# Optimization experiments

Hardware: AMD Instinct MI355X
Metric: run time of the kernel (lower is better)

The kernel has to match this reference:

```python
import jax, jax.numpy as jnp
import numpy as np

# --- Cl(3,0,1) projective geometric algebra structure constants (GATr blade order) ---
BLADES = [(), (0,), (1,), (2,), (3,), (0, 1), (0, 2), (0, 3), (1, 2), (1, 3), (2, 3),
          (0, 1, 2), (0, 1, 3), (0, 2, 3), (1, 2, 3), (0, 1, 2, 3)]
IDX = {b: i for i, b in enumerate(BLADES)}
METRIC = [0.0, 1.0, 1.0, 1.0]  # e0 degenerate, e1,e2,e3 square to +1


def _mul_blades(a, b):
    """Multiply two basis blades; returns (sign, sorted_blade_tuple)."""
    lst = list(a) + list(b)
    sign = 1.0
    changed = True
    while changed:
        changed = False
        k = 0
        while k < len(lst) - 1:
            if lst[k] > lst[k + 1]:
                lst[k], lst[k + 1] = lst[k + 1], lst[k]
                sign = -sign
                changed = True
            elif lst[k] == lst[k + 1]:
                sign *= METRIC[lst[k]]
                del lst[k:k + 2]
                changed = True
            else:
                k += 1
    return sign, tuple(lst)


def _tables():
    gp = np.zeros((16, 16, 16), np.float32)
    outer = np.zeros((16, 16, 16), np.float32)
    for j, bj in enumerate(BLADES):
        for k, bk in enumerate(BLADES):
            s, bl = _mul_blades(bj, bk)
            if s != 0.0:
                gp[IDX[bl], j, k] = s
            if set(bj).isdisjoint(bk):  # outer product: nonzero only for disjoint blades
                outer[IDX[bl], j, k] = s
    # dual map D: blade -> signed complement, with blade ^ complement = sign * e0123
    D = np.zeros((16, 16), np.float32)
    for j, bj in enumerate(BLADES):
        comp = tuple(i for i in range(4) if i not in bj)
        s, _ = _mul_blades(bj, comp)
        D[IDX[comp], j] = s
    # join(x, y) = dual(dual(x) ^ dual(y))  ->  bilinear tensor [16,16,16]
    join = np.einsum('ai,ijk,jb,kc->abc', D, outer, D, D).astype(np.float32)
    # Pin-equivariant linear basis: 5 grade projections + 4 e0-wedge-per-grade maps
    grades = np.array([len(b) for b in BLADES])
    basis = np.zeros((9, 16, 16), np.float32)
    for g in range(5):
        basis[g] = np.diag((grades == g).astype(np.float32))
    e0_mul = outer[:, IDX[(0,)], :]  # x -> e0 ^ x
    for g in range(4):
        basis[5 + g] = e0_mul * (grades == g)[None, :].astype(np.float32)
    return gp, join, basis


B, N = 8, 4096
IN_MV, HID, OUT_MV = 32, 32, 32
HALF = HID // 2
IN_S, OUT_S = 64, 64
NB = 9


def setup_inputs() -> dict:
    key = jax.random.key(0)
    ks = jax.random.split(key, 16)
    gp, jn, basis = _tables()

    def wmv(k, o, i):
        return jax.random.normal(k, (o, i, NB), jnp.float32) / np.sqrt(i * NB)

    def ws(k, o, i):
        return jax.random.normal(k, (o, i), jnp.float32) / np.sqrt(i)

    return dict(
        multivectors=jax.random.normal(ks[0], (B, N, IN_MV, 16), jnp.float32),
        reference_mv=jax.random.normal(ks[1], (B, N, 16), jnp.float32),
        scalars=jax.random.normal(ks[2], (B, N, IN_S), jnp.float32),
        basis=jnp.asarray(basis), gp=jnp.asarray(gp), jn=jnp.asarray(jn),
        w_left_mv=wmv(ks[3], HALF, IN_MV), w_left_s=ws(ks[4], HALF, IN_S),
        w_right_mv=wmv(ks[5], HALF, IN_MV), w_right_s=ws(ks[6], HALF, IN_S),
        w_jl_mv=wmv(ks[7], HALF, IN_MV), w_jl_s=ws(ks[8], HALF, IN_S),
        w_jr_mv=wmv(ks[9], HALF, IN_MV), w_jr_s=ws(ks[10], HALF, IN_S),
        w_out_mv=wmv(ks[11], OUT_MV, HID), w_out_s2mv=ws(ks[12], OUT_MV, IN_S),
        w_out_mvs2s=ws(ks[13], OUT_S, HID), w_out_s2s=ws(ks[14], OUT_S, IN_S),
    )


def _equi_linear(x, s, w_mv, w_s, basis):
    # fold the 9 equivariant basis maps into the channel-mixing weight once (tiny)
    W = jnp.einsum('oib,bjk->oijk', w_mv, basis)  # [out, in, 16, 16]
    out = jnp.einsum('oijk,...ik->...oj', W, x)   # (..., out, 16)
    # scalar inputs feed the multivector scalar component (blade index 0)
    out = out.at[..., 0].add(jnp.einsum('os,...s->...o', w_s, s))
    return out


def reference(multivectors, reference_mv, scalars, basis, gp, jn,
              w_left_mv, w_left_s, w_right_mv, w_right_s, w_jl_mv, w_jl_s,
              w_jr_mv, w_jr_s, w_out_mv, w_out_s2mv, w_out_mvs2s, w_out_s2s):
    left = _equi_linear(multivectors, scalars, w_left_mv, w_left_s, basis)
    right = _equi_linear(multivectors, scalars, w_right_mv, w_right_s, basis)
    gp_out = jnp.einsum('ijk,...cj,...ck->...ci', gp, left, right)  # geometric product

    jl = _equi_linear(multivectors, scalars, w_jl_mv, w_jl_s, basis)
    jr = _equi_linear(multivectors, scalars, w_jr_mv, w_jr_s, basis)
    # equivariant join, scaled by pseudoscalar (e0123) component of the reference
    join_out = jnp.einsum('ijk,...cj,...ck->...ci', jn, jl, jr) * reference_mv[..., None, 15:16]

    hidden = jnp.concatenate([gp_out, join_out], axis=-2)  # (..., HID, 16)
    out_mv = _equi_linear(hidden, scalars, w_out_mv, w_out_s2mv, basis)
    out_s = jnp.einsum('oc,...c->...o', w_out_mvs2s, hidden[..., 0]) \
        + jnp.einsum('os,...s->...o', w_out_s2s, scalars)
    return out_mv, out_s
```

## Files before the change

kernel.cpp:

```cpp
#include <hip/hip_runtime.h>
#include <stdint.h>


#define NPOS_TOTAL 32768

typedef __attribute__((ext_vector_type(8))) short short8;
typedef __attribute__((ext_vector_type(4))) float f32x4;
#define MFMA16(a,b,c) __builtin_amdgcn_mfma_f32_16x16x32_bf16((a),(b),(c),0,0,0)

constexpr int BLADE_MASK[16] = {0,1,2,4,8,3,5,9,6,10,12,7,11,13,14,15};
constexpr int MASK2IDX[16]   = {0,1,2,5,3,6,8,11,4,7,9,12,10,13,14,15};

struct MulRes { int sign; int mask; };

constexpr MulRes mul_blades(int ma, int mb) {
  int lst[8] = {0,0,0,0,0,0,0,0};
  int n = 0;
  for (int g = 0; g < 4; ++g) if ((ma >> g) & 1) lst[n++] = g;
  for (int g = 0; g < 4; ++g) if ((mb >> g) & 1) lst[n++] = g;
  int sign = 1;
  bool changed = true;
  while (changed) {
    changed = false;
    int k = 0;
    while (k + 1 < n) {
      if (lst[k] > lst[k+1]) {
        int t = lst[k]; lst[k] = lst[k+1]; lst[k+1] = t;
        sign = -sign; changed = true;
      } else if (lst[k] == lst[k+1]) {
        if (lst[k] == 0) sign = 0;
        for (int m = k; m + 2 < n; ++m) lst[m] = lst[m+2];
        n -= 2; changed = true;
      } else {
        ++k;
      }
    }
  }
  int mask = 0;
  for (int m = 0; m < n; ++m) mask |= (1 << lst[m]);
  if (sign == 0) mask = 0;
  return MulRes{sign, mask};
}

struct Tables {
  float gp_sgn[16][16]; int gp_idx[16][16];
  float jn_sgn[16][16]; int jn_idx[16][16];
  constexpr Tables() : gp_sgn{}, gp_idx{}, jn_sgn{}, jn_idx{} {
    for (int j = 0; j < 16; ++j) {
      for (int k = 0; k < 16; ++k) {
        MulRes r = mul_blades(BLADE_MASK[j], BLADE_MASK[k]);
        gp_sgn[j][k] = (float)r.sign;
        gp_idx[j][k] = MASK2IDX[r.mask & 15];
        jn_sgn[j][k] = 0.0f; jn_idx[j][k] = 0;
        int mb = BLADE_MASK[j], mc = BLADE_MASK[k];
        if ((mb | mc) == 15) {
          int cb = 15 ^ mb, cc = 15 ^ mc;
          MulRes sb = mul_blades(mb, cb);
          MulRes sc = mul_blades(mc, cc);
          MulRes ro = mul_blades(cb, cc);
          int imask = ro.mask;
          int amask = 15 ^ imask;
          MulRes si = mul_blades(imask, amask);
          jn_sgn[j][k] = (float)(si.sign * ro.sign * sb.sign * sc.sign);
          jn_idx[j][k] = MASK2IDX[amask & 15];
        }
      }
    }
  }
};
constexpr Tables TBL{};

constexpr int GRADE[16] = {0,1,1,1,1,2,2,2,2,2,2,3,3,3,3,4};
constexpr int E0_TGT[8]  = {1,5,6,7,11,12,13,15};
constexpr int E0_SRC[8]  = {0,2,3,4,8,9,10,14};
constexpr int E0_SLOT[8] = {5,6,6,6,7,7,7,8};

__device__ __forceinline__ float bflo(unsigned u) { return __uint_as_float(u << 16); }
__device__ __forceinline__ float bfhi(unsigned u) { return __uint_as_float(u & 0xffff0000u); }
__device__ __forceinline__ unsigned pk2(float a, float b) {
  unsigned ua = __float_as_uint(a), ub = __float_as_uint(b);
  unsigned ra = (ua + 0x7fffu + ((ua >> 16) & 1u)) >> 16;
  unsigned rb = (ub + 0x7fffu + ((ub >> 16) & 1u)) >> 16;
  return (ra & 0xffffu) | ((rb & 0xffffu) << 16);
}
__device__ __forceinline__ unsigned short bf1(float a) {
  unsigned ua = __float_as_uint(a);
  return (unsigned short)((ua + 0x7fffu + ((ua >> 16) & 1u)) >> 16);
}

__global__ void gb_prep(const float* __restrict__ wlmv, const float* __restrict__ wrmv,
                        const float* __restrict__ wjlmv, const float* __restrict__ wjrmv,
                        const float* __restrict__ wls,  const float* __restrict__ wrs,
                        const float* __restrict__ wjls, const float* __restrict__ wjrs,
                        const float* __restrict__ womv, const float* __restrict__ ws2mv,
                        const float* __restrict__ wm2s, const float* __restrict__ ws2s,
                        uint4* __restrict__ wpk) {
  int t = blockIdx.x * 256 + threadIdx.x;
  if (t >= 168 * 64) return;
  int blk = t >> 6, l = t & 63;
  int m = l & 15, q = l >> 4;
  float v[8];
  if (blk < 104) {
    int mat = blk >> 2, ot = blk & 3;
    const float* wmv[4] = {wlmv, wrmv, wjlmv, wjrmv};
    const float* wsc[4] = {wls, wrs, wjls, wjrs};
    for (int jj = 0; jj < 8; ++jj) {
      int k = q * 8 + jj;
      if (mat < 16)      v[jj] = wmv[ot][m * 288 + k * 9 + GRADE[mat]];
      else if (mat < 24) v[jj] = wmv[ot][m * 288 + k * 9 + E0_SLOT[mat - 16]];
      else               v[jj] = wsc[ot][m * 64 + (mat - 24) * 32 + k];
    }
  } else if (blk < 156) {
    int b2 = blk - 104, mat = b2 >> 1, ot = b2 & 1;
    int o = ot * 16 + m;
    for (int jj = 0; jj < 8; ++jj) {
      int k = q * 8 + jj;
      if (mat < 16)      v[jj] = womv[o * 288 + k * 9 + GRADE[mat]];
      else if (mat < 24) v[jj] = womv[o * 288 + k * 9 + E0_SLOT[mat - 16]];
      else               v[jj] = ws2mv[o * 64 + (mat - 24) * 32 + k];
    }
  } else {
    int b4 = blk - 156;
    for (int jj = 0; jj < 8; ++jj) {
      int k = q * 8 + jj;
      if (b4 < 4) { int o = b4 * 16 + m; v[jj] = wm2s[o * 32 + k]; }
      else { int half = (b4 - 4) >> 2, ot = (b4 - 4) & 3; int o = ot * 16 + m;
             v[jj] = ws2s[o * 64 + half * 32 + k]; }
    }
  }
  uint4 u;
  u.x = pk2(v[0], v[1]); u.y = pk2(v[2], v[3]);
  u.z = pk2(v[4], v[5]); u.w = pk2(v[6], v[7]);
  wpk[t] = u;
}

__global__ __launch_bounds__(256) void gb_main(
    const float* __restrict__ mv, const float* __restrict__ ref,
    const float* __restrict__ s, const uint4* __restrict__ wpk,
    float* __restrict__ out_mv, float* __restrict__ out_s) {
  __shared__ __align__(16) char smem[57600];
  unsigned short* xs_e = (unsigned short*)smem;
  unsigned*       xs_w = (unsigned*)smem;
  unsigned short* hl_e = (unsigned short*)smem;
  unsigned short* yl_e = (unsigned short*)(smem + 16640);
  unsigned*       yl_w = (unsigned*)(smem + 16640);

  const int tid  = threadIdx.x;
  const int wave = tid >> 6, lane = tid & 63;
  const int lm = lane & 15, lq = lane >> 4;
  const int P0 = blockIdx.x * 16;

  const float4* mv4 = (const float4*)mv + (size_t)P0 * 128;
  #pragma unroll
  for (int kk = 0; kk < 4; ++kk) {
    int e = tid + kk * 256;
    int p = e >> 6, sub = e & 63, i2 = sub >> 2, jg = sub & 3;
    float4 fa = mv4[p * 128 + i2 * 8 + jg];
    float4 fb = mv4[p * 128 + i2 * 8 + 4 + jg];
    int base = p * 260 + jg * 4 * 16 + i2;
    xs_w[base + 0 * 16] = pk2(fa.x, fb.x);
    xs_w[base + 1 * 16] = pk2(fa.y, fb.y);
    xs_w[base + 2 * 16] = pk2(fa.z, fb.z);
    xs_w[base + 3 * 16] = pk2(fa.w, fb.w);
  }

  short8 sfrag[2];
  {
    const float4* s4 = (const float4*)s + ((size_t)(P0 + lm)) * 16;
    #pragma unroll
    for (int h = 0; h < 2; ++h) {
      float4 a = s4[h * 8 + lq * 2];
      float4 b = s4[h * 8 + lq * 2 + 1];
      uint4 u;
      u.x = pk2(a.x, a.y); u.y = pk2(a.z, a.w);
      u.z = pk2(b.x, b.y); u.w = pk2(b.z, b.w);
      sfrag[h] = __builtin_bit_cast(short8, u);
    }
  }
  __syncthreads();

  {
    short8 bx[16];
    #pragma unroll
    for (int c = 0; c < 16; ++c)
      bx[c] = *(const short8*)&xs_e[lm * 520 + c * 32 + lq * 8];
    f32x4 zf = {0.f, 0.f, 0.f, 0.f};
    f32x4 acc[16];
    #pragma unroll
    for (int j = 0; j < 16; ++j) acc[j] = zf;
    #pragma unroll
    for (int j = 0; j < 16; ++j) {
      short8 w = __builtin_bit_cast(short8, wpk[(j * 4 + wave) * 64 + lane]);
      acc[j] = MFMA16(w, bx[j], acc[j]);
    }
    #pragma unroll
    for (int m = 0; m < 8; ++m) {
      short8 w = __builtin_bit_cast(short8, wpk[((16 + m) * 4 + wave) * 64 + lane]);
      acc[E0_TGT[m]] = MFMA16(w, bx[E0_SRC[m]], acc[E0_TGT[m]]);
    }
    #pragma unroll
    for (int h = 0; h < 2; ++h) {
      short8 w = __builtin_bit_cast(short8, wpk[((24 + h) * 4 + wave) * 64 + lane]);
      acc[0] = MFMA16(w, sfrag[h], acc[0]);
    }
    #pragma unroll
    for (int jp = 0; jp < 8; ++jp) {
      #pragma unroll
      for (int r = 0; r < 4; ++r) {
        int o = wave * 16 + lq * 4 + r;
        yl_w[o * 160 + lm * 10 + jp] = pk2(acc[2 * jp][r], acc[2 * jp + 1][r]);
      }
    }
  }
  __syncthreads();

  {
    const int pos = tid & 15;
    const int hc  = tid >> 4;
    const float rs = ref[(size_t)(P0 + pos) * 16 + 15];
    float L[16], R[16], H[16];
    auto ldrow = [&](int row, float* dst) {
      const unsigned short* p = yl_e + row * 320 + pos * 20;
      uint2 a = *(const uint2*)(p);
      uint2 b = *(const uint2*)(p + 4);
      uint2 c = *(const uint2*)(p + 8);
      uint2 d = *(const uint2*)(p + 12);
      unsigned uu[8] = {a.x, a.y, b.x, b.y, c.x, c.y, d.x, d.y};
      #pragma unroll
      for (int q = 0; q < 8; ++q) { dst[2*q] = bflo(uu[q]); dst[2*q+1] = bfhi(uu[q]); }
    };
    ldrow(hc, L); ldrow(16 + hc, R);
    #pragma unroll
    for (int q = 0; q < 16; ++q) H[q] = 0.f;
    #pragma unroll
    for (int j = 0; j < 16; ++j)
      #pragma unroll
      for (int k = 0; k < 16; ++k)
        if (TBL.gp_sgn[j][k] != 0.0f)
          H[TBL.gp_idx[j][k]] += TBL.gp_sgn[j][k] * L[j] * R[k];
    #pragma unroll
    for (int j = 0; j < 16; ++j)
      hl_e[pos * 520 + j * 32 + hc] = bf1(H[j]);
    ldrow(32 + hc, L); ldrow(48 + hc, R);
    #pragma unroll
    for (int q = 0; q < 16; ++q) { H[q] = 0.f; L[q] *= rs; }
    #pragma unroll
    for (int j = 0; j < 16; ++j)
      #pragma unroll
      for (int k = 0; k < 16; ++k)
        if (TBL.jn_sgn[j][k] != 0.0f)
          H[TBL.jn_idx[j][k]] += TBL.jn_sgn[j][k] * L[j] * R[k];
    #pragma unroll
    for (int j = 0; j < 16; ++j)
      hl_e[pos * 520 + j * 32 + 16 + hc] = bf1(H[j]);
  }
  __syncthreads();

  if (wave < 2) {
    short8 bh[16];
    #pragma unroll
    for (int j = 0; j < 16; ++j)
      bh[j] = *(const short8*)&hl_e[lm * 520 + j * 32 + lq * 8];
    f32x4 zf = {0.f, 0.f, 0.f, 0.f};
    f32x4 a3[16];
    #pragma unroll
    for (int j = 0; j < 16; ++j) a3[j] = zf;
    #pragma unroll
    for (int j = 0; j < 16; ++j) {
      short8 w = __builtin_bit_cast(short8, wpk[(104 + j * 2 + wave) * 64 + lane]);
      a3[j] = MFMA16(w, bh[j], a3[j]);
    }
    #pragma unroll
    for (int m = 0; m < 8; ++m) {
      short8 w = __builtin_bit_cast(short8, wpk[(104 + (16 + m) * 2 + wave) * 64 + lane]);
      a3[E0_TGT[m]] = MFMA16(w, bh[E0_SRC[m]], a3[E0_TGT[m]]);
    }
    #pragma unroll
    for (int h = 0; h < 2; ++h) {
      short8 w = __builtin_bit_cast(short8, wpk[(104 + (24 + h) * 2 + wave) * 64 + lane]);
      a3[0] = MFMA16(w, sfrag[h], a3[0]);
    }
    float* ob = out_mv + ((size_t)(P0 + lm)) * 512 + (size_t)(wave * 16 + lq * 4) * 16;
    #pragma unroll
    for (int r = 0; r < 4; ++r) {
      #pragma unroll
      for (int g = 0; g < 4; ++g) {
        *(float4*)(ob + r * 16 + g * 4) =
            make_float4(a3[4*g][r], a3[4*g+1][r], a3[4*g+2][r], a3[4*g+3][r]);
      }
    }
  } else {
    short8 bh0 = *(const short8*)&hl_e[lm * 520 + lq * 8];
    int w2 = wave - 2;
    f32x4 zf = {0.f, 0.f, 0.f, 0.f};
    #pragma unroll
    for (int t2 = 0; t2 < 2; ++t2) {
      int otg = w2 * 2 + t2;
      f32x4 aS = zf;
      aS = MFMA16(__builtin_bit_cast(short8, wpk[(156 + otg) * 64 + lane]), bh0, aS);
      aS = MFMA16(__builtin_bit_cast(short8, wpk[(160 + otg) * 64 + lane]), sfrag[0], aS);
      aS = MFMA16(__builtin_bit_cast(short8, wpk[(164 + otg) * 64 + lane]), sfrag[1], aS);
      float* osb = out_s + ((size_t)(P0 + lm)) * 64 + otg * 16 + lq * 4;
      *(float4*)osb = make_float4(aS[0], aS[1], aS[2], aS[3]);
    }
  }
}

extern "C" void kernel_launch(void* const* d_in, const int* in_sizes, int n_in,
                              void* d_out, int out_size, void* d_ws, size_t ws_size,
                              hipStream_t stream) {
  (void)in_sizes; (void)n_in; (void)out_size; (void)ws_size;
  const float* mv    = (const float*)d_in[0];
  const float* ref   = (const float*)d_in[1];
  const float* s     = (const float*)d_in[2];
  const float* wlmv  = (const float*)d_in[6];
  const float* wls   = (const float*)d_in[7];
  const float* wrmv  = (const float*)d_in[8];
  const float* wrs   = (const float*)d_in[9];
  const float* wjlmv = (const float*)d_in[10];
  const float* wjls  = (const float*)d_in[11];
  const float* wjrmv = (const float*)d_in[12];
  const float* wjrs  = (const float*)d_in[13];
  const float* womv  = (const float*)d_in[14];
  const float* ws2mv = (const float*)d_in[15];
  const float* wm2s  = (const float*)d_in[16];
  const float* ws2s  = (const float*)d_in[17];

  float* out_mv = (float*)d_out;
  float* out_s  = out_mv + (size_t)NPOS_TOTAL * 32 * 16;
  uint4* wpk = (uint4*)d_ws;

  gb_prep<<<42, 256, 0, stream>>>(wlmv, wrmv, wjlmv, wjrmv, wls, wrs, wjls, wjrs,
                                  womv, ws2mv, wm2s, ws2s, wpk);
  gb_main<<<NPOS_TOTAL / 16, 256, 0, stream>>>(mv, ref, s, wpk, out_mv, out_s);
}
```

Baseline: 191.9 us.

## Load input fragments directly to registers and shrink shared memory for higher occupancy

The input multivectors are now read from global memory straight into MFMA B-fragment registers instead of being staged through LDS, which removes one barrier and the LDS round trip. The hidden-layer LDS buffer is now aliased onto the same region after an added barrier, with padded layouts and vectorised uint2 stores. Together with the smaller footprint (~41.5KB vs 57.6KB), launch_bounds(256,3) asks for three blocks per CU, trading register pressure for occupancy. The global reads per lane become strided (each lane reads its own position row), which may lower coalescing.

```diff
diff --git a/kernel.cpp b/kernel.cpp
--- a/kernel.cpp
+++ b/kernel.cpp
@@ -88,6 +88,11 @@
   return (unsigned short)((ua + 0x7fffu + ((ua >> 16) & 1u)) >> 16);
 }
 
+__device__ __forceinline__ int YL(int o, int pos, int jp) {
+  return o * 162 + (o >> 4) * 8 + pos * 10 + jp;
+}
+#define HL_U32(pos, j, ch2) ((pos) * 272 + (j) * 16 + (ch2))
+
 __global__ void gb_prep(const float* __restrict__ wlmv, const float* __restrict__ wrmv,
                         const float* __restrict__ wjlmv, const float* __restrict__ wjrmv,
                         const float* __restrict__ wls,  const float* __restrict__ wrs,
@@ -134,34 +139,41 @@
   wpk[t] = u;
 }
 
-__global__ __launch_bounds__(256) void gb_main(
+__global__ __launch_bounds__(256, 3) void gb_main(
     const float* __restrict__ mv, const float* __restrict__ ref,
     const float* __restrict__ s, const uint4* __restrict__ wpk,
     float* __restrict__ out_mv, float* __restrict__ out_s) {
-  __shared__ __align__(16) char smem[57600];
-  unsigned short* xs_e = (unsigned short*)smem;
-  unsigned*       xs_w = (unsigned*)smem;
-  unsigned short* hl_e = (unsigned short*)smem;
-  unsigned short* yl_e = (unsigned short*)(smem + 16640);
-  unsigned*       yl_w = (unsigned*)(smem + 16640);
+  __shared__ __align__(16) unsigned smem_u32[10392];
+  unsigned short* smem_us = (unsigned short*)smem_u32;
 
   const int tid  = threadIdx.x;
   const int wave = tid >> 6, lane = tid & 63;
   const int lm = lane & 15, lq = lane >> 4;
   const int P0 = blockIdx.x * 16;
 
-  const float4* mv4 = (const float4*)mv + (size_t)P0 * 128;
-  #pragma unroll
-  for (int kk = 0; kk < 4; ++kk) {
-    int e = tid + kk * 256;
-    int p = e >> 6, sub = e & 63, i2 = sub >> 2, jg = sub & 3;
-    float4 fa = mv4[p * 128 + i2 * 8 + jg];
-    float4 fb = mv4[p * 128 + i2 * 8 + 4 + jg];
-    int base = p * 260 + jg * 4 * 16 + i2;
-    xs_w[base + 0 * 16] = pk2(fa.x, fb.x);
-    xs_w[base + 1 * 16] = pk2(fa.y, fb.y);
-    xs_w[base + 2 * 16] = pk2(fa.z, fb.z);
-    xs_w[base + 3 * 16] = pk2(fa.w, fb.w);
+  uint4 bxu[16];
+  {
+    const float4* xb = (const float4*)(mv + (size_t)(P0 + lm) * 512 + lq * 128);
+    #pragma unroll
+    for (int p = 0; p < 4; ++p) {
+      float4 A[4], B[4];
+      #pragma unroll
+      for (int q = 0; q < 4; ++q) { A[q] = xb[p * 8 + q]; B[q] = xb[p * 8 + 4 + q]; }
+      float af[16], bf[16];
+      #pragma unroll
+      for (int q = 0; q < 4; ++q) {
+        af[q*4+0] = A[q].x; af[q*4+1] = A[q].y; af[q*4+2] = A[q].z; af[q*4+3] = A[q].w;
+        bf[q*4+0] = B[q].x; bf[q*4+1] = B[q].y; bf[q*4+2] = B[q].z; bf[q*4+3] = B[q].w;
+      }
+      #pragma unroll
+      for (int j = 0; j < 16; ++j) {
+        unsigned u = pk2(af[j], bf[j]);
+        if      (p == 0) bxu[j].x = u;
+        else if (p == 1) bxu[j].y = u;
+        else if (p == 2) bxu[j].z = u;
+        else             bxu[j].w = u;
+      }
+    }
   }
 
   short8 sfrag[2];
@@ -177,13 +189,8 @@
       sfrag[h] = __builtin_bit_cast(short8, u);
     }
   }
-  __syncthreads();
-
-  {
-    short8 bx[16];
-    #pragma unroll
-    for (int c = 0; c < 16; ++c)
-      bx[c] = *(const short8*)&xs_e[lm * 520 + c * 32 + lq * 8];
+
+  {
     f32x4 zf = {0.f, 0.f, 0.f, 0.f};
     f32x4 acc[16];
     #pragma unroll
@@ -191,12 +198,12 @@
     #pragma unroll
     for (int j = 0; j < 16; ++j) {
       short8 w = __builtin_bit_cast(short8, wpk[(j * 4 + wave) * 64 + lane]);
-      acc[j] = MFMA16(w, bx[j], acc[j]);
+      acc[j] = MFMA16(w, __builtin_bit_cast(short8, bxu[j]), acc[j]);
     }
     #pragma unroll
     for (int m = 0; m < 8; ++m) {
       short8 w = __builtin_bit_cast(short8, wpk[((16 + m) * 4 + wave) * 64 + lane]);
-      acc[E0_TGT[m]] = MFMA16(w, bx[E0_SRC[m]], acc[E0_TGT[m]]);
+      acc[E0_TGT[m]] = MFMA16(w, __builtin_bit_cast(short8, bxu[E0_SRC[m]]), acc[E0_TGT[m]]);
     }
     #pragma unroll
     for (int h = 0; h < 2; ++h) {
@@ -204,32 +211,43 @@
       acc[0] = MFMA16(w, sfrag[h], acc[0]);
     }
     #pragma unroll
-    for (int jp = 0; jp < 8; ++jp) {
-      #pragma unroll
-      for (int r = 0; r < 4; ++r) {
-        int o = wave * 16 + lq * 4 + r;
-        yl_w[o * 160 + lm * 10 + jp] = pk2(acc[2 * jp][r], acc[2 * jp + 1][r]);
+    for (int r = 0; r < 4; ++r) {
+      int o = wave * 16 + lq * 4 + r;
+      int base = YL(o, lm, 0);
+      #pragma unroll
+      for (int jp2 = 0; jp2 < 4; ++jp2) {
+        uint2 v;
+        v.x = pk2(acc[4*jp2 + 0][r], acc[4*jp2 + 1][r]);
+        v.y = pk2(acc[4*jp2 + 2][r], acc[4*jp2 + 3][r]);
+        *(uint2*)&smem_u32[base + jp2 * 2] = v;
       }
     }
   }
   __syncthreads();
 
-  {
-    const int pos = tid & 15;
-    const int hc  = tid >> 4;
-    const float rs = ref[(size_t)(P0 + pos) * 16 + 15];
-    float L[16], R[16], H[16];
-    auto ldrow = [&](int row, float* dst) {
-      const unsigned short* p = yl_e + row * 320 + pos * 20;
-      uint2 a = *(const uint2*)(p);
-      uint2 b = *(const uint2*)(p + 4);
-      uint2 c = *(const uint2*)(p + 8);
-      uint2 d = *(const uint2*)(p + 12);
-      unsigned uu[8] = {a.x, a.y, b.x, b.y, c.x, c.y, d.x, d.y};
-      #pragma unroll
-      for (int q = 0; q < 8; ++q) { dst[2*q] = bflo(uu[q]); dst[2*q+1] = bfhi(uu[q]); }
-    };
-    ldrow(hc, L); ldrow(16 + hc, R);
+  const int pos = tid & 15;
+  const int hc  = tid >> 4;
+  float Lr[16], Rr[16], Jl[16], Jr[16];
+  {
+    float* dsts[4] = {Lr, Rr, Jl, Jr};
+    #pragma unroll
+    for (int mrow = 0; mrow < 4; ++mrow) {
+      int row = mrow * 16 + hc;
+      int base = YL(row, pos, 0);
+      float* dst = dsts[mrow];
+      #pragma unroll
+      for (int jp2 = 0; jp2 < 4; ++jp2) {
+        uint2 v = *(const uint2*)&smem_u32[base + jp2 * 2];
+        dst[4*jp2 + 0] = bflo(v.x); dst[4*jp2 + 1] = bfhi(v.x);
+        dst[4*jp2 + 2] = bflo(v.y); dst[4*jp2 + 3] = bfhi(v.y);
+      }
+    }
+  }
+  const float rs = ref[(size_t)(P0 + pos) * 16 + 15];
+  __syncthreads();
+
+  {
+    float H[16];
     #pragma unroll
     for (int q = 0; q < 16; ++q) H[q] = 0.f;
     #pragma unroll
@@ -237,43 +255,41 @@
       #pragma unroll
       for (int k = 0; k < 16; ++k)
         if (TBL.gp_sgn[j][k] != 0.0f)
-          H[TBL.gp_idx[j][k]] += TBL.gp_sgn[j][k] * L[j] * R[k];
+          H[TBL.gp_idx[j][k]] += TBL.gp_sgn[j][k] * Lr[j] * Rr[k];
     #pragma unroll
     for (int j = 0; j < 16; ++j)
-      hl_e[pos * 520 + j * 32 + hc] = bf1(H[j]);
-    ldrow(32 + hc, L); ldrow(48 + hc, R);
-    #pragma unroll
-    for (int q = 0; q < 16; ++q) { H[q] = 0.f; L[q] *= rs; }
+      smem_us[pos * 544 + j * 32 + hc] = bf1(H[j]);
+
+    #pragma unroll
+    for (int q = 0; q < 16; ++q) { H[q] = 0.f; Jl[q] *= rs; }
     #pragma unroll
     for (int j = 0; j < 16; ++j)
       #pragma unroll
       for (int k = 0; k < 16; ++k)
         if (TBL.jn_sgn[j][k] != 0.0f)
-          H[TBL.jn_idx[j][k]] += TBL.jn_sgn[j][k] * L[j] * R[k];
+          H[TBL.jn_idx[j][k]] += TBL.jn_sgn[j][k] * Jl[j] * Jr[k];
     #pragma unroll
     for (int j = 0; j < 16; ++j)
-      hl_e[pos * 520 + j * 32 + 16 + hc] = bf1(H[j]);
+      smem_us[pos * 544 + j * 32 + 16 + hc] = bf1(H[j]);
   }
   __syncthreads();
 
   if (wave < 2) {
-    short8 bh[16];
-    #pragma unroll
-    for (int j = 0; j < 16; ++j)
-      bh[j] = *(const short8*)&hl_e[lm * 520 + j * 32 + lq * 8];
     f32x4 zf = {0.f, 0.f, 0.f, 0.f};
     f32x4 a3[16];
     #pragma unroll
     for (int j = 0; j < 16; ++j) a3[j] = zf;
     #pragma unroll
     for (int j = 0; j < 16; ++j) {
+      uint4 hv = *(const uint4*)&smem_u32[HL_U32(lm, j, lq * 4)];
       short8 w = __builtin_bit_cast(short8, wpk[(104 + j * 2 + wave) * 64 + lane]);
-      a3[j] = MFMA16(w, bh[j], a3[j]);
+      a3[j] = MFMA16(w, __builtin_bit_cast(short8, hv), a3[j]);
     }
     #pragma unroll
     for (int m = 0; m < 8; ++m) {
+      uint4 hv = *(const uint4*)&smem_u32[HL_U32(lm, E0_SRC[m], lq * 4)];
       short8 w = __builtin_bit_cast(short8, wpk[(104 + (16 + m) * 2 + wave) * 64 + lane]);
-      a3[E0_TGT[m]] = MFMA16(w, bh[E0_SRC[m]], a3[E0_TGT[m]]);
+      a3[E0_TGT[m]] = MFMA16(w, __builtin_bit_cast(short8, hv), a3[E0_TGT[m]]);
     }
     #pragma unroll
     for (int h = 0; h < 2; ++h) {
@@ -290,7 +306,8 @@
       }
     }
   } else {
-    short8 bh0 = *(const short8*)&hl_e[lm * 520 + lq * 8];
+    uint4 hv0 = *(const uint4*)&smem_u32[HL_U32(lm, 0, lq * 4)];
+    short8 bh0 = __builtin_bit_cast(short8, hv0);
     int w2 = wave - 2;
     f32x4 zf = {0.f, 0.f, 0.f, 0.f};
     #pragma unroll
```

Result: slower. 228.8 us (+19.2%).
